# Kernel optimization log

Measured on AMD Instinct MI355X. Metric: run time of the kernel, lower is better.

Reference implementation:

```python
import jax, jax.numpy as jnp
import numpy as np

N, E = 50000, 800000
IN_F, HID, OUT_F, K = 128, 128, 64, 3
LAMBDA_MAX = 2.0  # standard upper bound for normalized-Laplacian eigenvalues (dgl.laplacian_lambda_max)
BN_EPS = 1e-5


def setup_inputs() -> dict:
    key = jax.random.key(0)
    ks = jax.random.split(key, 8)
    s = 0.05
    features = jax.random.normal(ks[0], (N, IN_F), jnp.float32)
    src = jax.random.randint(ks[1], (E,), 0, N)
    dst = jax.random.randint(ks[2], (E,), 0, N)
    W1 = jax.random.normal(ks[3], (HID, K * IN_F), jnp.float32) * s
    b1 = jnp.zeros((HID,), jnp.float32)
    W3 = jax.random.normal(ks[4], (HID, K * HID), jnp.float32) * s
    b3 = jnp.zeros((HID,), jnp.float32)
    gamma = jnp.ones((HID,), jnp.float32)
    beta = jnp.zeros((HID,), jnp.float32)
    Wm1 = jax.random.normal(ks[5], (HID, HID), jnp.float32) * s
    bm1 = jnp.zeros((HID,), jnp.float32)
    Wm2 = jax.random.normal(ks[6], (OUT_F, HID), jnp.float32) * s
    bm2 = jnp.zeros((OUT_F,), jnp.float32)
    return dict(features=features, src=src, dst=dst, W1=W1, b1=b1, W3=W3, b3=b3,
                gamma=gamma, beta=beta, Wm1=Wm1, bm1=bm1, Wm2=Wm2, bm2=bm2)


def chebconv(feat, src, dst, d_invsqrt, W, b, k):
    """DGL ChebConv: T_0 = X, T_1 = Lhat X, T_i = 2 Lhat T_{i-1} - T_{i-2};
    Lhat = (2/lam) (I - Ahat) - I, Ahat = D^{-1/2} A D^{-1/2}; linear over concat of orders."""
    re_norm = 2.0 / LAMBDA_MAX
    n = feat.shape[0]

    def spmv(x):  # Ahat @ x via edge gather (src) + segment-sum scatter (dst)
        return jax.ops.segment_sum((x * d_invsqrt)[src], dst, num_segments=n) * d_invsqrt

    Xs = [feat]
    if k > 1:
        h = spmv(feat)
        Xs.append(-re_norm * h + feat * (re_norm - 1.0))
    for _ in range(2, k):
        h = spmv(Xs[-1])
        Xs.append(-2.0 * re_norm * h + Xs[-1] * (2.0 * (re_norm - 1.0)) - Xs[-2])
    return jnp.concatenate(Xs, axis=1) @ W.T + b  # [N, k*d] @ [d_out, k*d]^T


def reference(features, src, dst, W1, b1, W3, b3, gamma, beta, Wm1, bm1, Wm2, bm2):
    n = features.shape[0]
    in_deg = jax.ops.segment_sum(jnp.ones((src.shape[0],), jnp.float32), dst, num_segments=n)
    d_invsqrt = (jnp.clip(in_deg, 1.0, None) ** -0.5)[:, None]

    x = jax.nn.relu(chebconv(features, src, dst, d_invsqrt, W1, b1, K))
    # BatchNorm1d (training-mode batch stats, biased variance)
    mu = x.mean(axis=0)
    var = x.var(axis=0)
    x = (x - mu) * jax.lax.rsqrt(var + BN_EPS) * gamma + beta
    # NOTE: the source's Chebyshev early-stopping loop computes cheb2(x) repeatedly but
    # never reassigns `x`, so it is output-inert and omitted (same math).
    x_res = x
    x = jax.nn.relu(chebconv(x, src, dst, d_invsqrt, W3, b3, K))
    x = x + x_res  # dropout in eval mode == identity
    h = jax.nn.relu(x @ Wm1.T + bm1)
    return h @ Wm2.T + bm2
```

## Files before the change

### kernel.cpp

```cpp
#include <hip/hip_runtime.h>
#include <hip/hip_bf16.h>
#include <math.h>

#define NF 128

typedef unsigned short ushort8 __attribute__((ext_vector_type(8)));
typedef float f32x4 __attribute__((ext_vector_type(4)));
typedef _Float16 half8 __attribute__((ext_vector_type(8)));

static inline int ceil_div(int a, int b) { return (a + b - 1) / b; }

__global__ __launch_bounds__(256) void bucket_hist_kernel(const int* __restrict__ dst,
                                                          int* __restrict__ counts,
                                                          int e, int nblk, int nbuck) {
  __shared__ int h[256];
  int t = threadIdx.x, blk = blockIdx.x;
  h[t] = 0;
  __syncthreads();
  int base = blk * 4096;
#pragma unroll
  for (int k = 0; k < 16; ++k) {
    int i = base + k * 256 + t;
    if (i < e) atomicAdd(&h[dst[i] >> 8], 1);
  }
  __syncthreads();
  for (int b = t; b < nbuck; b += 256) counts[b * nblk + blk] = h[b];
}

__global__ __launch_bounds__(256) void bucket_scan_rows_kernel(int* __restrict__ counts,
                                                               int* __restrict__ btot,
                                                               int nblk) {
  __shared__ int sh[256];
  int b = blockIdx.x, t = threadIdx.x;
  int* row = counts + (size_t)b * nblk;
  int carry = 0;
  for (int base = 0; base < nblk; base += 256) {
    int v = (base + t < nblk) ? row[base + t] : 0;
    sh[t] = v;
    __syncthreads();
    for (int off = 1; off < 256; off <<= 1) {
      int add = (t >= off) ? sh[t - off] : 0;
      __syncthreads();
      sh[t] += add;
      __syncthreads();
    }
    if (base + t < nblk) row[base + t] = carry + sh[t] - v;
    carry += sh[255];
    __syncthreads();
  }
  if (t == 0) btot[b] = carry;
}

__global__ __launch_bounds__(256) void bucket_base_kernel(const int* __restrict__ btot,
                                                          int* __restrict__ bbase,
                                                          int nbuck, int e) {
  __shared__ int sh[256];
  __shared__ int carry;
  int t = threadIdx.x;
  if (t == 0) carry = 0;
  __syncthreads();
  for (int base = 0; base < nbuck; base += 256) {
    int v = (base + t < nbuck) ? btot[base + t] : 0;
    sh[t] = v;
    __syncthreads();
    for (int off = 1; off < 256; off <<= 1) {
      int add = (t >= off) ? sh[t - off] : 0;
      __syncthreads();
      sh[t] += add;
      __syncthreads();
    }
    if (base + t < nbuck) bbase[base + t] = carry + sh[t] - v;
    __syncthreads();
    if (t == 0) carry += sh[255];
    __syncthreads();
  }
  if (t == 0) bbase[nbuck] = e;
}

__global__ __launch_bounds__(256) void bucket_bin_kernel(const int* __restrict__ src,
                                                         const int* __restrict__ dst,
                                                         const int* __restrict__ counts,
                                                         const int* __restrict__ bbase,
                                                         unsigned int* __restrict__ binned,
                                                         int e, int nblk, int nbuck) {
  __shared__ int cur[256];
  int t = threadIdx.x, blk = blockIdx.x;
  for (int b = t; b < nbuck; b += 256) cur[b] = counts[b * nblk + blk] + bbase[b];
  __syncthreads();
  int base = blk * 4096;
#pragma unroll
  for (int k = 0; k < 16; ++k) {
    int i = base + k * 256 + t;
    if (i < e) {
      int d = dst[i];
      int pos = atomicAdd(&cur[d >> 8], 1);
      binned[pos] = ((unsigned)(d & 255) << 16) | (unsigned)src[i];
    }
  }
}

__global__ __launch_bounds__(256) void bucket_finalize_kernel(const unsigned int* __restrict__ binned,
                                                              const int* __restrict__ bbase,
                                                              int* __restrict__ offsets,
                                                              int* __restrict__ csr,
                                                              float* __restrict__ dinv,
                                                              int n, int e, int nbuck) {
  __shared__ int deg[256];
  __shared__ int offs[256];
  __shared__ int cur[256];
  int b = blockIdx.x, t = threadIdx.x;
  int ebeg = bbase[b];
  int eend = bbase[b + 1];
  deg[t] = 0;
  __syncthreads();
  for (int j = ebeg + t; j < eend; j += 256) atomicAdd(&deg[binned[j] >> 16], 1);
  __syncthreads();
  int v = deg[t];
  offs[t] = v;
  __syncthreads();
  for (int off = 1; off < 256; off <<= 1) {
    int add = (t >= off) ? offs[t - off] : 0;
    __syncthreads();
    offs[t] += add;
    __syncthreads();
  }
  int excl = offs[t] - v;
  cur[t] = excl;
  int node = b * 256 + t;
  if (node < n) {
    offsets[node] = ebeg + excl;
    float d = (float)(v > 1 ? v : 1);
    dinv[node] = rsqrtf(d);
  }
  if (b == nbuck - 1 && t == 0) offsets[n] = e;
  __syncthreads();
  for (int j = ebeg + t; j < eend; j += 256) {
    unsigned int pr = binned[j];
    int pos = atomicAdd(&cur[pr >> 16], 1);
    csr[ebeg + pos] = (int)(pr & 0xFFFFu);
  }
}


__global__ void prep_feat_kernel(const float* __restrict__ feat,
                                 _Float16* __restrict__ Fsp, int n) {
  int i = blockIdx.x * 256 + threadIdx.x;
  if (i >= n * 16) return;
  int row = i >> 4, fc = i & 15;
  const float4* s = (const float4*)(feat + (size_t)row * NF + fc * 8);
  float4 a = s[0], b = s[1];
  float xv[8] = {a.x, a.y, a.z, a.w, b.x, b.y, b.z, b.w};
  half8 f;
#pragma unroll
  for (int j = 0; j < 8; ++j) f[j] = (_Float16)xv[j];
  int swz = (fc ^ (row & 15)) * 8;
  *(half8*)(Fsp + (size_t)row * 128 + swz) = f;
}

__global__ __launch_bounds__(256) void spmv_kernel(
    const _Float16* __restrict__ xsp, const float* __restrict__ dinv,
    const int* __restrict__ offsets, const int* __restrict__ csr,
    const _Float16* __restrict__ zsp, float a, float bz,
    _Float16* __restrict__ outsp, int n) {
  int w = threadIdx.x >> 6, lane = threadIdx.x & 63;
  int node = blockIdx.x * 4 + w;
  if (node >= n) return;
  int beg = __builtin_amdgcn_readfirstlane(offsets[node]);
  int end = __builtin_amdgcn_readfirstlane(offsets[node + 1]);
  int eh = lane >> 4;
  int cq = lane & 15;

  float acc[8];
#pragma unroll
  for (int j = 0; j < 8; ++j) acc[j] = 0.f;

  int e2 = beg;
  for (; e2 + 8 <= end; e2 += 8) {
    int s0 = csr[e2 + eh];
    int s1 = csr[e2 + 4 + eh];
    float w0 = dinv[s0], w1 = dinv[s1];
    half8 g0 = *(const half8*)(xsp + (size_t)s0 * 128 + ((cq ^ (s0 & 15)) << 3));
    half8 g1 = *(const half8*)(xsp + (size_t)s1 * 128 + ((cq ^ (s1 & 15)) << 3));
#pragma unroll
    for (int j = 0; j < 8; ++j) acc[j] += w0 * (float)g0[j];
#pragma unroll
    for (int j = 0; j < 8; ++j) acc[j] += w1 * (float)g1[j];
  }
  for (; e2 + 4 <= end; e2 += 4) {
    int s0 = csr[e2 + eh];
    float w0 = dinv[s0];
    half8 g0 = *(const half8*)(xsp + (size_t)s0 * 128 + ((cq ^ (s0 & 15)) << 3));
#pragma unroll
    for (int j = 0; j < 8; ++j) acc[j] += w0 * (float)g0[j];
  }
  int rem = end - e2;
  if (eh < rem) {
    int s0 = csr[e2 + eh];
    float w0 = dinv[s0];
    half8 g0 = *(const half8*)(xsp + (size_t)s0 * 128 + ((cq ^ (s0 & 15)) << 3));
#pragma unroll
    for (int j = 0; j < 8; ++j) acc[j] += w0 * (float)g0[j];
  }
#pragma unroll
  for (int j = 0; j < 8; ++j) {
    acc[j] += __shfl_xor(acc[j], 16);
    acc[j] += __shfl_xor(acc[j], 32);
  }
  if (eh == 0) {
    float dv = a * dinv[node];
    float v[8];
#pragma unroll
    for (int j = 0; j < 8; ++j) v[j] = dv * acc[j];
    int swz = (cq ^ (node & 15)) << 3;
    if (zsp) {
      half8 zz = *(const half8*)(zsp + (size_t)node * 128 + swz);
#pragma unroll
      for (int j = 0; j < 8; ++j) v[j] += bz * (float)zz[j];
    }
    half8 ho;
#pragma unroll
    for (int j = 0; j < 8; ++j) ho[j] = (_Float16)v[j];
    *(half8*)(outsp + (size_t)node * 128 + swz) = ho;
  }
}

__device__ __forceinline__ void pack_one(const float* __restrict__ W, ushort8* __restrict__ Wp,
                                         int f, int NT, int K, int rot) {
  int lane = f & 63;
  int hl = (f >> 6) & 1;
  int rest = f >> 7;
  int nt = rest % NT;
  int kunit = rest / NT;
  int nK = K >> 5;
  int srcKunit = (kunit + rot) % nK;
  int nrow = nt * 16 + (lane & 15);
  int k0 = srcKunit * 32 + (lane >> 4) * 8;
  const float* srcp = W + (size_t)nrow * K + k0;
  ushort8 v;
#pragma unroll
  for (int j = 0; j < 8; ++j) {
    float x = srcp[j];
    _Float16 h = (_Float16)x;
    if (hl) h = (_Float16)(x - (float)h);
    v[j] = __builtin_bit_cast(unsigned short, h);
  }
  Wp[f] = v;
}

__global__ void pack_all_kernel(const float* __restrict__ W1, ushort8* __restrict__ P1,
                                const float* __restrict__ W3, ushort8* __restrict__ P3,
                                const float* __restrict__ Wm1, ushort8* __restrict__ PM1,
                                const float* __restrict__ Wm2, ushort8* __restrict__ PM2) {
  int f = blockIdx.x * 256 + threadIdx.x;
  if (f < 12288) pack_one(W1, P1, f, 8, 384, 0);
  else if (f < 24576) pack_one(W3, P3, f - 12288, 8, 384, 4);
  else if (f < 28672) pack_one(Wm1, PM1, f - 24576, 8, 128, 0);
  else if (f < 30720) pack_one(Wm2, PM2, f - 28672, 4, 128, 0);
}


__device__ __forceinline__ void stage_sp(const _Float16* gsrc, float4* lbuf, int tid) {
  const char* g = (const char*)gsrc;
  char* l = (char*)lbuf;
#pragma unroll
  for (int k = 0; k < 2; ++k) {
    int off = k * 8192 + tid * 16;
    __builtin_amdgcn_global_load_lds(
        (const __attribute__((address_space(1))) void*)(g + off),
        (__attribute__((address_space(3))) void*)(l + off), 16, 0, 0);
  }
}

__device__ __forceinline__ int lds_off16(int row, int col) {
  return row * 128 + (((col >> 3) ^ (row & 15)) << 3) + (col & 7);
}

struct Bchunk {
  ushort8 h[2][2];
  ushort8 l[2][2];
};

__device__ __forceinline__ void loadB(const ushort8* __restrict__ Wp, int kunit0,
                                      int lane, int wn, Bchunk& c) {
#pragma unroll
  for (int k2 = 0; k2 < 2; ++k2) {
#pragma unroll
    for (int j = 0; j < 2; ++j) {
      const ushort8* bp = Wp + (size_t)((kunit0 + k2) * 8 + wn * 2 + j) * 128 + lane;
      c.h[k2][j] = bp[0];
      c.l[k2][j] = bp[64];
    }
  }
}

__device__ __forceinline__ void mfma_chunk(const float4* A4, const Bchunk& c, int kbase,
                                           int lane, int wm, f32x4 (*acc)[2]) {
#pragma unroll
  for (int k2 = 0; k2 < 2; ++k2) {
    int kunit = kbase + k2;
    half8 a[2];
#pragma unroll
    for (int mt = 0; mt < 2; ++mt) {
      int arow = wm * 32 + mt * 16 + (lane & 15);
      int fc = (kunit & 3) * 4 + (lane >> 4);
      a[mt] = __builtin_bit_cast(half8, A4[arow * 16 + (fc ^ (arow & 15))]);
    }
#pragma unroll
    for (int j = 0; j < 2; ++j) {
      half8 bh = __builtin_bit_cast(half8, c.h[k2][j]);
      half8 bl = __builtin_bit_cast(half8, c.l[k2][j]);
#pragma unroll
      for (int mt = 0; mt < 2; ++mt) {
        acc[mt][j] = __builtin_amdgcn_mfma_f32_16x16x32_f16(a[mt], bh, acc[mt][j], 0, 0, 0);
        acc[mt][j] = __builtin_amdgcn_mfma_f32_16x16x32_f16(a[mt], bl, acc[mt][j], 0, 0, 0);
      }
    }
  }
}

template<int NT, int NT2>
__device__ __forceinline__ void gemm_step16(const float4* A4, const ushort8* __restrict__ Wp,
                                            int kunit, int lane, int wm, int wn,
                                            f32x4 (*acc)[NT2]) {
  half8 a[2];
#pragma unroll
  for (int mt = 0; mt < 2; ++mt) {
    int arow = wm * 32 + mt * 16 + (lane & 15);
    int fc = (kunit & 3) * 4 + (lane >> 4);
    a[mt] = __builtin_bit_cast(half8, A4[arow * 16 + (fc ^ (arow & 15))]);
  }
#pragma unroll
  for (int j = 0; j < NT2; ++j) {
    int nt = wn * NT2 + j;
    const ushort8* bp = Wp + (size_t)(kunit * NT + nt) * 2 * 64 + lane;
    half8 bh = __builtin_bit_cast(half8, bp[0]);
    half8 bl = __builtin_bit_cast(half8, bp[64]);
#pragma unroll
    for (int mt = 0; mt < 2; ++mt) {
      acc[mt][j] = __builtin_amdgcn_mfma_f32_16x16x32_f16(a[mt], bh, acc[mt][j], 0, 0, 0);
      acc[mt][j] = __builtin_amdgcn_mfma_f32_16x16x32_f16(a[mt], bl, acc[mt][j], 0, 0, 0);
    }
  }
}

__device__ __forceinline__ void gemm3_pipeline(const _Float16* A0, const _Float16* A1,
                                               const _Float16* A2, const ushort8* Wp,
                                               float4 (*buf)[1024], size_t r0,
                                               int tid, int lane, int wm, int wn,
                                               f32x4 (*acc)[2]) {
  const _Float16* Aarr[3] = {A0, A1, A2};
  stage_sp(A0 + r0 * 128, buf[0], tid);
  Bchunk bc0, bc1;
#pragma unroll
  for (int p = 0; p < 3; ++p) {
    loadB(Wp, p * 4, lane, wn, bc0);
    loadB(Wp, p * 4 + 2, lane, wn, bc1);
    if (p + 1 < 3) stage_sp(Aarr[p + 1] + r0 * 128, buf[(p + 1) & 1], tid);
    asm volatile("s_waitcnt vmcnt(10)" ::: "memory");
    __builtin_amdgcn_s_barrier();
    __builtin_amdgcn_sched_barrier(0);
    mfma_chunk(buf[p & 1], bc0, p * 4, lane, wm, acc);
    mfma_chunk(buf[p & 1], bc1, p * 4 + 2, lane, wm, acc);
    __builtin_amdgcn_sched_barrier(0);
    __builtin_amdgcn_s_barrier();
  }
}

__global__ __launch_bounds__(512, 4) void conv1_gemm_kernel(
    const _Float16* __restrict__ A0, const _Float16* __restrict__ A1,
    const _Float16* __restrict__ A2,
    const ushort8* __restrict__ Wp, const float* __restrict__ bias,
    _Float16* __restrict__ Xsp, float* __restrict__ stats, int n) {
  __shared__ float4 buf[2][1024];
  __shared__ float sstat[256];

  int tid = threadIdx.x;
  int lane = tid & 63, wid = tid >> 6;
  int wm = wid >> 2, wn = wid & 3;
  size_t r0 = (size_t)blockIdx.x * 64;

  f32x4 acc[2][2];
#pragma unroll
  for (int mt = 0; mt < 2; ++mt)
#pragma unroll
    for (int j = 0; j < 2; ++j) acc[mt][j] = (f32x4)0.f;

  gemm3_pipeline(A0, A1, A2, Wp, buf, r0, tid, lane, wm, wn, acc);

  if (tid < 256) sstat[tid] = 0.f;
  __syncthreads();
#pragma unroll
  for (int mt = 0; mt < 2; ++mt) {
    int rbase = (int)r0 + wm * 32 + mt * 16 + (lane >> 4) * 4;
#pragma unroll
    for (int j = 0; j < 2; ++j) {
      int col = wn * 32 + j * 16 + (lane & 15);
      float b = bias[col];
      float sj = 0.f, qj = 0.f;
#pragma unroll
      for (int i = 0; i < 4; ++i) {
        int row = rbase + i;
        if (row < n) {
          float v = fmaxf(acc[mt][j][i] + b, 0.f);
          Xsp[(size_t)row * 128 + (((col >> 3) ^ (row & 15)) << 3) + (col & 7)] = (_Float16)v;
          sj += v; qj += v * v;
        }
      }
      sj += __shfl_xor(sj, 16); sj += __shfl_xor(sj, 32);
      qj += __shfl_xor(qj, 16); qj += __shfl_xor(qj, 32);
      if ((lane >> 4) == 0) {
        atomicAdd(&sstat[col], sj);
        atomicAdd(&sstat[128 + col], qj);
      }
    }
  }
  __syncthreads();
  if (tid < 256) atomicAdd(&stats[(blockIdx.x & 7) * 256 + tid], sstat[tid]);
}

__global__ __launch_bounds__(512, 4) void fused_tail_kernel(
    const _Float16* __restrict__ T1sp, const _Float16* __restrict__ T2sp,
    const _Float16* __restrict__ Xsp,
    const ushort8* __restrict__ Wp3, const float* __restrict__ b3,
    const ushort8* __restrict__ WpM1, const float* __restrict__ bm1,
    const ushort8* __restrict__ WpM2, const float* __restrict__ bm2,
    float* __restrict__ out, int n) {
  __shared__ float4 buf[2][1024];
  _Float16* L = (_Float16*)buf[0];

  int tid = threadIdx.x;
  int lane = tid & 63, wid = tid >> 6;
  int wm = wid >> 2, wn = wid & 3;
  size_t r0 = (size_t)blockIdx.x * 64;

  f32x4 acc[2][2];
#pragma unroll
  for (int mt = 0; mt < 2; ++mt)
#pragma unroll
    for (int j = 0; j < 2; ++j) acc[mt][j] = (f32x4)0.f;

  gemm3_pipeline(T1sp, T2sp, Xsp, Wp3, buf, r0, tid, lane, wm, wn, acc);

#pragma unroll
  for (int mt = 0; mt < 2; ++mt) {
    int rb = wm * 32 + mt * 16 + (lane >> 4) * 4;
#pragma unroll
    for (int j = 0; j < 2; ++j) {
      int col = wn * 32 + j * 16 + (lane & 15);
      float b = b3[col];
#pragma unroll
      for (int i = 0; i < 4; ++i) {
        int lrow = rb + i;
        int off = lds_off16(lrow, col);
        float xres = (float)L[off];
        float v = fmaxf(acc[mt][j][i] + b, 0.f) + xres;
        L[off] = (_Float16)v;
      }
    }
  }
  __syncthreads();
  f32x4 acc2[2][2];
#pragma unroll
  for (int mt = 0; mt < 2; ++mt)
#pragma unroll
    for (int j = 0; j < 2; ++j) acc2[mt][j] = (f32x4)0.f;
#pragma unroll
  for (int ks = 0; ks < 4; ++ks)
    gemm_step16<8, 2>(buf[0], WpM1, ks, lane, wm, wn, acc2);
  __syncthreads();
#pragma unroll
  for (int mt = 0; mt < 2; ++mt) {
    int rb = wm * 32 + mt * 16 + (lane >> 4) * 4;
#pragma unroll
    for (int j = 0; j < 2; ++j) {
      int col = wn * 32 + j * 16 + (lane & 15);
      float b = bm1[col];
#pragma unroll
      for (int i = 0; i < 4; ++i) {
        float v = fmaxf(acc2[mt][j][i] + b, 0.f);
        L[lds_off16(rb + i, col)] = (_Float16)v;
      }
    }
  }
  __syncthreads();
  f32x4 acc3[2][1];
#pragma unroll
  for (int mt = 0; mt < 2; ++mt) acc3[mt][0] = (f32x4)0.f;
#pragma unroll
  for (int ks = 0; ks < 4; ++ks)
    gemm_step16<4, 1>(buf[0], WpM2, ks, lane, wm, wn, acc3);
#pragma unroll
  for (int mt = 0; mt < 2; ++mt) {
    int rb = wm * 32 + mt * 16 + (lane >> 4) * 4;
    int col = wn * 16 + (lane & 15);
    float b = bm2[col];
#pragma unroll
    for (int i = 0; i < 4; ++i) {
      int row = (int)r0 + rb + i;
      if (row < n) out[(size_t)row * 64 + col] = acc3[mt][0][i] + b;
    }
  }
}

__global__ void bn_apply_kernel(_Float16* __restrict__ Xsp, const float* __restrict__ stats,
                                const float* __restrict__ gamma, const float* __restrict__ beta,
                                float fn, int n) {
  int i = blockIdx.x * 256 + threadIdx.x;
  if (i >= n * 16) return;
  int row = i >> 4, fc = i & 15;
  int swz = (fc ^ (row & 15)) * 8;
  half8* xp = (half8*)(Xsp + (size_t)row * 128 + swz);
  half8 xh = *xp;
  half8 hu;
  int c0 = fc * 8;
#pragma unroll
  for (int j = 0; j < 8; ++j) {
    int c = c0 + j;
    float s1 = 0.f, s2 = 0.f;
#pragma unroll
    for (int r = 0; r < 8; ++r) {
      s1 += stats[r * 256 + c];
      s2 += stats[r * 256 + NF + c];
    }
    float mu = s1 / fn;
    float var = s2 / fn - mu * mu;
    float s = gamma[c] * rsqrtf(var + 1e-5f);
    hu[j] = (_Float16)(((float)xh[j] - mu) * s + beta[c]);
  }
  *xp = hu;
}

extern "C" void kernel_launch(void* const* d_in, const int* in_sizes, int n_in,
                              void* d_out, int out_size, void* d_ws, size_t ws_size,
                              hipStream_t stream) {
  const float* feat  = (const float*)d_in[0];
  const int*   src   = (const int*)d_in[1];
  const int*   dst   = (const int*)d_in[2];
  const float* W1    = (const float*)d_in[3];
  const float* b1    = (const float*)d_in[4];
  const float* W3    = (const float*)d_in[5];
  const float* b3    = (const float*)d_in[6];
  const float* gamma = (const float*)d_in[7];
  const float* beta  = (const float*)d_in[8];
  const float* Wm1   = (const float*)d_in[9];
  const float* bm1   = (const float*)d_in[10];
  const float* Wm2   = (const float*)d_in[11];
  const float* bm2   = (const float*)d_in[12];
  int n = in_sizes[0] / NF;
  int e = in_sizes[1];

  char* p = (char*)d_ws;
  auto alloc = [&](size_t bytes) {
    char* r = p;
    p += (bytes + 255) & ~size_t(255);
    return r;
  };
  int nblk  = ceil_div(e, 4096);
  int nbuck = ceil_div(n, 256);

  float* dinv     = (float*)alloc((size_t)n * 4);
  int*   offsets  = (int*)alloc((size_t)(n + 1) * 4);
  int*   counts   = (int*)alloc((size_t)nblk * nbuck * 4);
  int*   btot     = (int*)alloc((size_t)nbuck * 4);
  int*   bbase    = (int*)alloc((size_t)(nbuck + 1) * 4);
  int*   csr      = (int*)alloc((size_t)e * 4);
  float* stats    = (float*)alloc(8 * 256 * 4);
  ushort8* Wp1  = (ushort8*)alloc(12 * 8 * 2 * 64 * 16);
  ushort8* Wp3  = (ushort8*)alloc(12 * 8 * 2 * 64 * 16);
  ushort8* WpM1 = (ushort8*)alloc(4 * 8 * 2 * 64 * 16);
  ushort8* WpM2 = (ushort8*)alloc(4 * 4 * 2 * 64 * 16);
  size_t spb = (size_t)(n + 64) * 256;
  _Float16* Fsp  = (_Float16*)alloc(spb);
  _Float16* T1sp = (_Float16*)alloc(spb);
  _Float16* T2sp = (_Float16*)alloc(spb);
  _Float16* Xsp  = (_Float16*)alloc(spb);
  unsigned int* binned = (unsigned int*)Fsp;

  hipMemsetAsync(stats, 0, 8 * 256 * 4, stream);

  int fb = ceil_div(n * 16, 256);
  int sb = ceil_div(n, 4);
  int gb = ceil_div(n, 64);

  bucket_hist_kernel<<<nblk, 256, 0, stream>>>(dst, counts, e, nblk, nbuck);
  bucket_scan_rows_kernel<<<nbuck, 256, 0, stream>>>(counts, btot, nblk);
  bucket_base_kernel<<<1, 256, 0, stream>>>(btot, bbase, nbuck, e);
  bucket_bin_kernel<<<nblk, 256, 0, stream>>>(src, dst, counts, bbase, binned, e, nblk, nbuck);
  bucket_finalize_kernel<<<nbuck, 256, 0, stream>>>(binned, bbase, offsets, csr, dinv, n, e, nbuck);

  pack_all_kernel<<<120, 256, 0, stream>>>(W1, Wp1, W3, Wp3, Wm1, WpM1, Wm2, WpM2);

  prep_feat_kernel<<<fb, 256, 0, stream>>>(feat, Fsp, n);
  spmv_kernel<<<sb, 256, 0, stream>>>(Fsp, dinv, offsets, csr, nullptr, -1.f, 0.f, T1sp, n);
  spmv_kernel<<<sb, 256, 0, stream>>>(T1sp, dinv, offsets, csr, Fsp, -2.f, -1.f, T2sp, n);
  conv1_gemm_kernel<<<gb, 512, 0, stream>>>(Fsp, T1sp, T2sp, Wp1, b1, Xsp, stats, n);

  bn_apply_kernel<<<fb, 256, 0, stream>>>(Xsp, stats, gamma, beta, (float)n, n);

  spmv_kernel<<<sb, 256, 0, stream>>>(Xsp, dinv, offsets, csr, nullptr, -1.f, 0.f, T1sp, n);
  spmv_kernel<<<sb, 256, 0, stream>>>(T1sp, dinv, offsets, csr, Xsp, -2.f, -1.f, T2sp, n);

  fused_tail_kernel<<<gb, 512, 0, stream>>>(T1sp, T2sp, Xsp, Wp3, b3, WpM1, bm1,
                                            WpM2, bm2, (float*)d_out, n);
}
```

Before: 254.1 us.

## Fold bucket base scan into consumers, merge prep and pack, single-stage GEMM staging

Drops the single-block bucket_base kernel: bucket_bin and bucket_finalize now each redo the small bucket-total prefix scan in shared memory. The feature fp16 conversion and the weight packing move into one combined launch. The three-operand GEMM stops double-buffering and stages all three A tiles into a 48KB LDS region up front, then interleaves B loads with MFMA chunks. Together these cut kernel launches and pipeline barriers, at the cost of redundant scans, a per-block scan that only handles up to 256 buckets, and higher LDS use per block that can lower occupancy.

New measurement: 251.7 us. Within noise of the previous version (-0.9%).

```diff
diff --git a/kernel.cpp b/kernel.cpp
--- a/kernel.cpp
+++ b/kernel.cpp
@@ -51,41 +51,25 @@
   if (t == 0) btot[b] = carry;
 }
 
-__global__ __launch_bounds__(256) void bucket_base_kernel(const int* __restrict__ btot,
-                                                          int* __restrict__ bbase,
-                                                          int nbuck, int e) {
-  __shared__ int sh[256];
-  __shared__ int carry;
-  int t = threadIdx.x;
-  if (t == 0) carry = 0;
-  __syncthreads();
-  for (int base = 0; base < nbuck; base += 256) {
-    int v = (base + t < nbuck) ? btot[base + t] : 0;
-    sh[t] = v;
-    __syncthreads();
-    for (int off = 1; off < 256; off <<= 1) {
-      int add = (t >= off) ? sh[t - off] : 0;
-      __syncthreads();
-      sh[t] += add;
-      __syncthreads();
-    }
-    if (base + t < nbuck) bbase[base + t] = carry + sh[t] - v;
-    __syncthreads();
-    if (t == 0) carry += sh[255];
-    __syncthreads();
-  }
-  if (t == 0) bbase[nbuck] = e;
-}
-
 __global__ __launch_bounds__(256) void bucket_bin_kernel(const int* __restrict__ src,
                                                          const int* __restrict__ dst,
                                                          const int* __restrict__ counts,
-                                                         const int* __restrict__ bbase,
+                                                         const int* __restrict__ btot,
                                                          unsigned int* __restrict__ binned,
                                                          int e, int nblk, int nbuck) {
+  __shared__ int sh[256];
   __shared__ int cur[256];
   int t = threadIdx.x, blk = blockIdx.x;
-  for (int b = t; b < nbuck; b += 256) cur[b] = counts[b * nblk + blk] + bbase[b];
+  int v = (t < nbuck) ? btot[t] : 0;
+  sh[t] = v;
+  __syncthreads();
+  for (int off = 1; off < 256; off <<= 1) {
+    int add = (t >= off) ? sh[t - off] : 0;
+    __syncthreads();
+    sh[t] += add;
+    __syncthreads();
+  }
+  if (t < nbuck) cur[t] = counts[(size_t)t * nblk + blk] + (sh[t] - v);
   __syncthreads();
   int base = blk * 4096;
 #pragma unroll
@@ -100,19 +84,30 @@
 }
 
 __global__ __launch_bounds__(256) void bucket_finalize_kernel(const unsigned int* __restrict__ binned,
-                                                              const int* __restrict__ bbase,
+                                                              const int* __restrict__ btot,
                                                               int* __restrict__ offsets,
                                                               int* __restrict__ csr,
                                                               float* __restrict__ dinv,
                                                               int n, int e, int nbuck) {
+  __shared__ int sh[256];
   __shared__ int deg[256];
   __shared__ int offs[256];
   __shared__ int cur[256];
+  __shared__ int sbeg, send;
   int b = blockIdx.x, t = threadIdx.x;
-  int ebeg = bbase[b];
-  int eend = bbase[b + 1];
+  int v0 = (t < nbuck) ? btot[t] : 0;
+  sh[t] = v0;
+  __syncthreads();
+  for (int off = 1; off < 256; off <<= 1) {
+    int add = (t >= off) ? sh[t - off] : 0;
+    __syncthreads();
+    sh[t] += add;
+    __syncthreads();
+  }
+  if (t == 0) { sbeg = (b > 0) ? sh[b - 1] : 0; send = sh[b]; }
   deg[t] = 0;
   __syncthreads();
+  int ebeg = sbeg, eend = send;
   for (int j = ebeg + t; j < eend; j += 256) atomicAdd(&deg[binned[j] >> 16], 1);
   __syncthreads();
   int v = deg[t];
@@ -141,88 +136,6 @@
   }
 }
 
-
-__global__ void prep_feat_kernel(const float* __restrict__ feat,
-                                 _Float16* __restrict__ Fsp, int n) {
-  int i = blockIdx.x * 256 + threadIdx.x;
-  if (i >= n * 16) return;
-  int row = i >> 4, fc = i & 15;
-  const float4* s = (const float4*)(feat + (size_t)row * NF + fc * 8);
-  float4 a = s[0], b = s[1];
-  float xv[8] = {a.x, a.y, a.z, a.w, b.x, b.y, b.z, b.w};
-  half8 f;
-#pragma unroll
-  for (int j = 0; j < 8; ++j) f[j] = (_Float16)xv[j];
-  int swz = (fc ^ (row & 15)) * 8;
-  *(half8*)(Fsp + (size_t)row * 128 + swz) = f;
-}
-
-__global__ __launch_bounds__(256) void spmv_kernel(
-    const _Float16* __restrict__ xsp, const float* __restrict__ dinv,
-    const int* __restrict__ offsets, const int* __restrict__ csr,
-    const _Float16* __restrict__ zsp, float a, float bz,
-    _Float16* __restrict__ outsp, int n) {
-  int w = threadIdx.x >> 6, lane = threadIdx.x & 63;
-  int node = blockIdx.x * 4 + w;
-  if (node >= n) return;
-  int beg = __builtin_amdgcn_readfirstlane(offsets[node]);
-  int end = __builtin_amdgcn_readfirstlane(offsets[node + 1]);
-  int eh = lane >> 4;
-  int cq = lane & 15;
-
-  float acc[8];
-#pragma unroll
-  for (int j = 0; j < 8; ++j) acc[j] = 0.f;
-
-  int e2 = beg;
-  for (; e2 + 8 <= end; e2 += 8) {
-    int s0 = csr[e2 + eh];
-    int s1 = csr[e2 + 4 + eh];
-    float w0 = dinv[s0], w1 = dinv[s1];
-    half8 g0 = *(const half8*)(xsp + (size_t)s0 * 128 + ((cq ^ (s0 & 15)) << 3));
-    half8 g1 = *(const half8*)(xsp + (size_t)s1 * 128 + ((cq ^ (s1 & 15)) << 3));
-#pragma unroll
-    for (int j = 0; j < 8; ++j) acc[j] += w0 * (float)g0[j];
-#pragma unroll
-    for (int j = 0; j < 8; ++j) acc[j] += w1 * (float)g1[j];
-  }
-  for (; e2 + 4 <= end; e2 += 4) {
-    int s0 = csr[e2 + eh];
-    float w0 = dinv[s0];
-    half8 g0 = *(const half8*)(xsp + (size_t)s0 * 128 + ((cq ^ (s0 & 15)) << 3));
-#pragma unroll
-    for (int j = 0; j < 8; ++j) acc[j] += w0 * (float)g0[j];
-  }
-  int rem = end - e2;
-  if (eh < rem) {
-    int s0 = csr[e2 + eh];
-    float w0 = dinv[s0];
-    half8 g0 = *(const half8*)(xsp + (size_t)s0 * 128 + ((cq ^ (s0 & 15)) << 3));
-#pragma unroll
-    for (int j = 0; j < 8; ++j) acc[j] += w0 * (float)g0[j];
-  }
-#pragma unroll
-  for (int j = 0; j < 8; ++j) {
-    acc[j] += __shfl_xor(acc[j], 16);
-    acc[j] += __shfl_xor(acc[j], 32);
-  }
-  if (eh == 0) {
-    float dv = a * dinv[node];
-    float v[8];
-#pragma unroll
-    for (int j = 0; j < 8; ++j) v[j] = dv * acc[j];
-    int swz = (cq ^ (node & 15)) << 3;
-    if (zsp) {
-      half8 zz = *(const half8*)(zsp + (size_t)node * 128 + swz);
-#pragma unroll
-      for (int j = 0; j < 8; ++j) v[j] += bz * (float)zz[j];
-    }
-    half8 ho;
-#pragma unroll
-    for (int j = 0; j < 8; ++j) ho[j] = (_Float16)v[j];
-    *(half8*)(outsp + (size_t)node * 128 + swz) = ho;
-  }
-}
 
 __device__ __forceinline__ void pack_one(const float* __restrict__ W, ushort8* __restrict__ Wp,
                                          int f, int NT, int K, int rot) {
@@ -247,15 +160,99 @@
   Wp[f] = v;
 }
 
-__global__ void pack_all_kernel(const float* __restrict__ W1, ushort8* __restrict__ P1,
-                                const float* __restrict__ W3, ushort8* __restrict__ P3,
-                                const float* __restrict__ Wm1, ushort8* __restrict__ PM1,
-                                const float* __restrict__ Wm2, ushort8* __restrict__ PM2) {
-  int f = blockIdx.x * 256 + threadIdx.x;
-  if (f < 12288) pack_one(W1, P1, f, 8, 384, 0);
-  else if (f < 24576) pack_one(W3, P3, f - 12288, 8, 384, 4);
-  else if (f < 28672) pack_one(Wm1, PM1, f - 24576, 8, 128, 0);
-  else if (f < 30720) pack_one(Wm2, PM2, f - 28672, 4, 128, 0);
+__global__ void prep_pack_kernel(const float* __restrict__ feat, _Float16* __restrict__ Fsp,
+                                 int n, int fb,
+                                 const float* __restrict__ W1, ushort8* __restrict__ P1,
+                                 const float* __restrict__ W3, ushort8* __restrict__ P3,
+                                 const float* __restrict__ Wm1, ushort8* __restrict__ PM1,
+                                 const float* __restrict__ Wm2, ushort8* __restrict__ PM2) {
+  int blk = blockIdx.x;
+  if (blk < fb) {
+    int i = blk * 256 + threadIdx.x;
+    if (i >= n * 16) return;
+    int row = i >> 4, fc = i & 15;
+    const float4* s = (const float4*)(feat + (size_t)row * NF + fc * 8);
+    float4 a = s[0], b = s[1];
+    float xv[8] = {a.x, a.y, a.z, a.w, b.x, b.y, b.z, b.w};
+    half8 f;
+#pragma unroll
+    for (int j = 0; j < 8; ++j) f[j] = (_Float16)xv[j];
+    int swz = (fc ^ (row & 15)) * 8;
+    *(half8*)(Fsp + (size_t)row * 128 + swz) = f;
+  } else {
+    int f = (blk - fb) * 256 + threadIdx.x;
+    if (f < 12288) pack_one(W1, P1, f, 8, 384, 0);
+    else if (f < 24576) pack_one(W3, P3, f - 12288, 8, 384, 4);
+    else if (f < 28672) pack_one(Wm1, PM1, f - 24576, 8, 128, 0);
+    else if (f < 30720) pack_one(Wm2, PM2, f - 28672, 4, 128, 0);
+  }
+}
+
+__global__ __launch_bounds__(256) void spmv_kernel(
+    const _Float16* __restrict__ xsp, const float* __restrict__ dinv,
+    const int* __restrict__ offsets, const int* __restrict__ csr,
+    const _Float16* __restrict__ zsp, float a, float bz,
+    _Float16* __restrict__ outsp, int n) {
+  int w = threadIdx.x >> 6, lane = threadIdx.x & 63;
+  int node = blockIdx.x * 4 + w;
+  if (node >= n) return;
+  int beg = __builtin_amdgcn_readfirstlane(offsets[node]);
+  int end = __builtin_amdgcn_readfirstlane(offsets[node + 1]);
+  int eh = lane >> 4;
+  int cq = lane & 15;
+
+  float acc[8];
+#pragma unroll
+  for (int j = 0; j < 8; ++j) acc[j] = 0.f;
+
+  int e2 = beg;
+  for (; e2 + 8 <= end; e2 += 8) {
+    int s0 = csr[e2 + eh];
+    int s1 = csr[e2 + 4 + eh];
+    float w0 = dinv[s0], w1 = dinv[s1];
+    half8 g0 = *(const half8*)(xsp + (size_t)s0 * 128 + ((cq ^ (s0 & 15)) << 3));
+    half8 g1 = *(const half8*)(xsp + (size_t)s1 * 128 + ((cq ^ (s1 & 15)) << 3));
+#pragma unroll
+    for (int j = 0; j < 8; ++j) acc[j] += w0 * (float)g0[j];
+#pragma unroll
+    for (int j = 0; j < 8; ++j) acc[j] += w1 * (float)g1[j];
+  }
+  for (; e2 + 4 <= end; e2 += 4) {
+    int s0 = csr[e2 + eh];
+    float w0 = dinv[s0];
+    half8 g0 = *(const half8*)(xsp + (size_t)s0 * 128 + ((cq ^ (s0 & 15)) << 3));
+#pragma unroll
+    for (int j = 0; j < 8; ++j) acc[j] += w0 * (float)g0[j];
+  }
+  int rem = end - e2;
+  if (eh < rem) {
+    int s0 = csr[e2 + eh];
+    float w0 = dinv[s0];
+    half8 g0 = *(const half8*)(xsp + (size_t)s0 * 128 + ((cq ^ (s0 & 15)) << 3));
+#pragma unroll
+    for (int j = 0; j < 8; ++j) acc[j] += w0 * (float)g0[j];
+  }
+#pragma unroll
+  for (int j = 0; j < 8; ++j) {
+    acc[j] += __shfl_xor(acc[j], 16);
+    acc[j] += __shfl_xor(acc[j], 32);
+  }
+  if (eh == 0) {
+    float dv = a * dinv[node];
+    float v[8];
+#pragma unroll
+    for (int j = 0; j < 8; ++j) v[j] = dv * acc[j];
+    int swz = (cq ^ (node & 15)) << 3;
+    if (zsp) {
+      half8 zz = *(const half8*)(zsp + (size_t)node * 128 + swz);
+#pragma unroll
+      for (int j = 0; j < 8; ++j) v[j] += bz * (float)zz[j];
+    }
+    half8 ho;
+#pragma unroll
+    for (int j = 0; j < 8; ++j) ho[j] = (_Float16)v[j];
+    *(half8*)(outsp + (size_t)node * 128 + swz) = ho;
+  }
 }
 
 
@@ -343,27 +340,30 @@
   }
 }
 
-__device__ __forceinline__ void gemm3_pipeline(const _Float16* A0, const _Float16* A1,
-                                               const _Float16* A2, const ushort8* Wp,
-                                               float4 (*buf)[1024], size_t r0,
-                                               int tid, int lane, int wm, int wn,
-                                               f32x4 (*acc)[2]) {
-  const _Float16* Aarr[3] = {A0, A1, A2};
-  stage_sp(A0 + r0 * 128, buf[0], tid);
+__device__ __forceinline__ void gemm3_single(const _Float16* A0, const _Float16* A1,
+                                             const _Float16* A2, const ushort8* Wp,
+                                             float4* lds, size_t r0,
+                                             int tid, int lane, int wm, int wn,
+                                             f32x4 (*acc)[2]) {
+  stage_sp(A0 + r0 * 128, lds, tid);
+  stage_sp(A1 + r0 * 128, lds + 1024, tid);
+  stage_sp(A2 + r0 * 128, lds + 2048, tid);
   Bchunk bc0, bc1;
-#pragma unroll
-  for (int p = 0; p < 3; ++p) {
-    loadB(Wp, p * 4, lane, wn, bc0);
-    loadB(Wp, p * 4 + 2, lane, wn, bc1);
-    if (p + 1 < 3) stage_sp(Aarr[p + 1] + r0 * 128, buf[(p + 1) & 1], tid);
-    asm volatile("s_waitcnt vmcnt(10)" ::: "memory");
-    __builtin_amdgcn_s_barrier();
-    __builtin_amdgcn_sched_barrier(0);
-    mfma_chunk(buf[p & 1], bc0, p * 4, lane, wm, acc);
-    mfma_chunk(buf[p & 1], bc1, p * 4 + 2, lane, wm, acc);
-    __builtin_amdgcn_sched_barrier(0);
-    __builtin_amdgcn_s_barrier();
-  }
+  loadB(Wp, 0, lane, wn, bc0);
+  asm volatile("s_waitcnt vmcnt(8)" ::: "memory");
+  __builtin_amdgcn_s_barrier();
+  __builtin_amdgcn_sched_barrier(0);
+  loadB(Wp, 2, lane, wn, bc1);
+  mfma_chunk(lds, bc0, 0, lane, wm, acc);
+  loadB(Wp, 4, lane, wn, bc0);
+  mfma_chunk(lds, bc1, 2, lane, wm, acc);
+  loadB(Wp, 6, lane, wn, bc1);
+  mfma_chunk(lds + 1024, bc0, 4, lane, wm, acc);
+  loadB(Wp, 8, lane, wn, bc0);
+  mfma_chunk(lds + 1024, bc1, 6, lane, wm, acc);
+  loadB(Wp, 10, lane, wn, bc1);
+  mfma_chunk(lds + 2048, bc0, 8, lane, wm, acc);
+  mfma_chunk(lds + 2048, bc1, 10, lane, wm, acc);
 }
 
 __global__ __launch_bounds__(512, 4) void conv1_gemm_kernel(
@@ -371,7 +371,7 @@
     const _Float16* __restrict__ A2,
     const ushort8* __restrict__ Wp, const float* __restrict__ bias,
     _Float16* __restrict__ Xsp, float* __restrict__ stats, int n) {
-  __shared__ float4 buf[2][1024];
+  __shared__ float4 lds[3072];
   __shared__ float sstat[256];
 
   int tid = threadIdx.x;
@@ -385,7 +385,7 @@
 #pragma unroll
     for (int j = 0; j < 2; ++j) acc[mt][j] = (f32x4)0.f;
 
-  gemm3_pipeline(A0, A1, A2, Wp, buf, r0, tid, lane, wm, wn, acc);
+  gemm3_single(A0, A1, A2, Wp, lds, r0, tid, lane, wm, wn, acc);
 
   if (tid < 256) sstat[tid] = 0.f;
   __syncthreads();
@@ -425,8 +425,9 @@
     const ushort8* __restrict__ WpM1, const float* __restrict__ bm1,
     const ushort8* __restrict__ WpM2, const float* __restrict__ bm2,
     float* __restrict__ out, int n) {
-  __shared__ float4 buf[2][1024];
-  _Float16* L = (_Float16*)buf[0];
+  __shared__ float4 lds[3072];
+  _Float16* L0 = (_Float16*)lds;
+  _Float16* LX = (_Float16*)(lds + 2048);
 
   int tid = threadIdx.x;
   int lane = tid & 63, wid = tid >> 6;
@@ -439,7 +440,8 @@
 #pragma unroll
     for (int j = 0; j < 2; ++j) acc[mt][j] = (f32x4)0.f;
 
-  gemm3_pipeline(T1sp, T2sp, Xsp, Wp3, buf, r0, tid, lane, wm, wn, acc);
+  gemm3_single(T1sp, T2sp, Xsp, Wp3, lds, r0, tid, lane, wm, wn, acc);
+  __syncthreads();
 
 #pragma unroll
   for (int mt = 0; mt < 2; ++mt) {
@@ -452,9 +454,9 @@
       for (int i = 0; i < 4; ++i) {
         int lrow = rb + i;
         int off = lds_off16(lrow, col);
-        float xres = (float)L[off];
+        float xres = (float)LX[off];
         float v = fmaxf(acc[mt][j][i] + b, 0.f) + xres;
-        L[off] = (_Float16)v;
+        L0[off] = (_Float16)v;
       }
     }
   }
@@ -466,7 +468,7 @@
     for (int j = 0; j < 2; ++j) acc2[mt][j] = (f32x4)0.f;
 #pragma unroll
   for (int ks = 0; ks < 4; ++ks)
-    gemm_step16<8, 2>(buf[0], WpM1, ks, lane, wm, wn, acc2);
+    gemm_step16<8, 2>(lds, WpM1, ks, lane, wm, wn, acc2);
   __syncthreads();
 #pragma unroll
   for (int mt = 0; mt < 2; ++mt) {
@@ -478,7 +480,7 @@
 #pragma unroll
       for (int i = 0; i < 4; ++i) {
         float v = fmaxf(acc2[mt][j][i] + b, 0.f);
-        L[lds_off16(rb + i, col)] = (_Float16)v;
+        L0[lds_off16(rb + i, col)] = (_Float16)v;
       }
     }
   }
@@ -488,7 +490,7 @@
   for (int mt = 0; mt < 2; ++mt) acc3[mt][0] = (f32x4)0.f;
 #pragma unroll
   for (int ks = 0; ks < 4; ++ks)
-    gemm_step16<4, 1>(buf[0], WpM2, ks, lane, wm, wn, acc3);
+    gemm_step16<4, 1>(lds, WpM2, ks, lane, wm, wn, acc3);
 #pragma unroll
   for (int mt = 0; mt < 2; ++mt) {
     int rb = wm * 32 + mt * 16 + (lane >> 4) * 4;
@@ -562,7 +564,6 @@
   int*   offsets  = (int*)alloc((size_t)(n + 1) * 4);
   int*   counts   = (int*)alloc((size_t)nblk * nbuck * 4);
   int*   btot     = (int*)alloc((size_t)nbuck * 4);
-  int*   bbase    = (int*)alloc((size_t)(nbuck + 1) * 4);
   int*   csr      = (int*)alloc((size_t)e * 4);
   float* stats    = (float*)alloc(8 * 256 * 4);
   ushort8* Wp1  = (ushort8*)alloc(12 * 8 * 2 * 64 * 16);
@@ -584,13 +585,12 @@
 
   bucket_hist_kernel<<<nblk, 256, 0, stream>>>(dst, counts, e, nblk, nbuck);
   bucket_scan_rows_kernel<<<nbuck, 256, 0, stream>>>(counts, btot, nblk);
-  bucket_base_kernel<<<1, 256, 0, stream>>>(btot, bbase, nbuck, e);
-  bucket_bin_kernel<<<nblk, 256, 0, stream>>>(src, dst, counts, bbase, binned, e, nblk, nbuck);
-  bucket_finalize_kernel<<<nbuck, 256, 0, stream>>>(binned, bbase, offsets, csr, dinv, n, e, nbuck);
-
-  pack_all_kernel<<<120, 256, 0, stream>>>(W1, Wp1, W3, Wp3, Wm1, WpM1, Wm2, WpM2);
-
-  prep_feat_kernel<<<fb, 256, 0, stream>>>(feat, Fsp, n);
+  bucket_bin_kernel<<<nblk, 256, 0, stream>>>(src, dst, counts, btot, binned, e, nblk, nbuck);
+  bucket_finalize_kernel<<<nbuck, 256, 0, stream>>>(binned, btot, offsets, csr, dinv, n, e, nbuck);
+
+  prep_pack_kernel<<<fb + 120, 256, 0, stream>>>(feat, Fsp, n, fb,
+                                                 W1, Wp1, W3, Wp3, Wm1, WpM1, Wm2, WpM2);
+
   spmv_kernel<<<sb, 256, 0, stream>>>(Fsp, dinv, offsets, csr, nullptr, -1.f, 0.f, T1sp, n);
   spmv_kernel<<<sb, 256, 0, stream>>>(T1sp, dinv, offsets, csr, Fsp, -2.f, -1.f, T2sp, n);
   conv1_gemm_kernel<<<gb, 512, 0, stream>>>(Fsp, T1sp, T2sp, Wp1, b1, Xsp, stats, n);
```
